# Optimization experiments

Hardware: AMD Instinct MI355X
Metric: run time of the kernel (lower is better)

The kernel has to match this reference:

```python
import jax, jax.numpy as jnp
import numpy as np


def _freq_downsample(x, sf):
    # torch: stack(chunk(dim=2), 4) -> cat(chunk(dim=3), 4) -> mean(-1) -> repeat(1,1,sf,sf)
    # equivalent: mean over the sf x sf grid of contiguous blocks, then tile back.
    B, C, H, W = x.shape
    m = x.reshape(B, C, sf, H // sf, sf, W // sf).mean(axis=(2, 4))
    return jnp.tile(m, (1, 1, sf, sf))


def setup_inputs() -> dict:
    key = jax.random.key(0)
    k1, k2, k3 = jax.random.split(key, 3)
    shape = (4, 3, 256, 256)
    return {
        "STy": jax.random.normal(k1, shape, dtype=jnp.float32),
        "Fk_real": jax.random.normal(k2, shape, dtype=jnp.float32),
        "Fk_imag": jax.random.normal(k3, shape, dtype=jnp.float32),
        "sf": 2,
    }


def _forward(STy, Fk_real, Fk_imag, sf, num_iters=50, alpha=1e-6, gam=0.1):
    fft2 = lambda a: jnp.fft.fft2(a, axes=(-2, -1))
    ifft2 = lambda a: jnp.fft.ifft2(a, axes=(-2, -1))

    Fk = jax.lax.complex(Fk_real, Fk_imag)          # complex64 OTF
    FkC = jnp.conj(Fk)
    Fk2 = Fk_real ** 2 + Fk_imag ** 2               # |Fk|^2, real

    FSTy = fft2(STy)
    Fr = FkC * FSTy / (_freq_downsample(Fk2, sf) + alpha)
    pred = ifft2(Fr).real

    # finite-difference stencils DH = [1,-1] horizontal, DV vertical
    DH = jnp.zeros_like(pred).at[..., 0, 0].set(1.0).at[..., 0, 1].set(-1.0)
    DV = jnp.zeros_like(pred).at[..., 0, 0].set(1.0).at[..., 1, 0].set(-1.0)
    FDH, FDV = fft2(DH), fft2(DV)
    FDHC, FDVC = jnp.conj(FDH), jnp.conj(FDV)
    FD2 = jnp.abs(FDV) ** 2 + jnp.abs(FDH) ** 2 + 1e-8  # real

    # loop-invariant terms (identical math to recomputing each iteration)
    den = _freq_downsample(Fk2 / FD2, sf) + alpha
    FkFSTy = FkC * FSTy

    def body(carry, k):
        pred, x_old, t_old, U1, U2, D1, D2 = carry
        gam_k = gam * jnp.exp2(-k / num_iters)      # gam * 0.5 ** (k/num_iters)
        Fr = FkFSTy + alpha * (FDHC * fft2(U1 - D1) + FDVC * fft2(U2 - D2))
        Fr = (Fr - FkC * _freq_downsample(Fk * Fr / FD2, sf) / den) / (alpha * FD2)
        x_new = ifft2(Fr).real
        t_new = (1.0 + jnp.sqrt(1.0 + 4.0 * t_old ** 2)) / 2.0
        pred = x_new + (t_old - 1.0) / t_new * (x_new - x_old)
        DHr = ifft2(Fr * FDH).real
        DVr = ifft2(Fr * FDV).real
        NU1, NU2 = DHr + D1, DVr + D2
        NU = jnp.sqrt(NU1 ** 2 + NU2 ** 2 + 1e-8)
        A = jnp.maximum(0.0, NU - gam_k) + 1e-8
        A = A / (A + gam_k)                         # soft-threshold magnitude shrink
        U1n, U2n = A * NU1, A * NU2
        return (pred, x_new, t_new, U1n, U2n, D1 + DHr - U1n, D2 + DVr - U2n), None

    carry0 = (pred, pred, jnp.float32(1.0), pred, pred,
              jnp.zeros_like(pred), jnp.zeros_like(pred))
    ks = jnp.arange(num_iters, dtype=jnp.float32)
    (pred, *_), _ = jax.lax.scan(body, carry0, ks)
    return pred


def reference(STy, Fk_real, Fk_imag, sf):
    return _forward(STy, Fk_real, Fk_imag, sf)
```

## Files before the change

kernel.cpp:

```cpp
#include <hip/hip_runtime.h>
#include <math.h>

#define NIMG 12
#define NSZ 256
#define HWSZ 65536

__device__ __forceinline__ void fft256(float2* A, float2* B, const float2* tw, int lane, float dir)
{
  float2* src = A;
  float2* dst = B;
  int m = 1;
#pragma unroll
  for (int s = 0; s < 8; ++s) {
    __syncthreads();
#pragma unroll
    for (int h = 0; h < 2; ++h) {
      int b = lane + (h << 6);
      int k = b & (m - 1);
      int jm = b - k;
      float2 a = src[b];
      float2 c = src[b + 128];
      float2 w = tw[jm];
      float wr = w.x, wi = dir * w.y;
      float ex = a.x - c.x, ey = a.y - c.y;
      dst[2 * jm + k]     = make_float2(a.x + c.x, a.y + c.y);
      dst[2 * jm + k + m] = make_float2(ex * wr - ey * wi, ex * wi + ey * wr);
    }
    float2* t = src; src = dst; dst = t;
    m <<= 1;
  }
  __syncthreads();
}

__device__ __forceinline__ void make_tw(float2* tw, int t)
{
  float s, c;
  sincospif((float)t * (1.0f / 128.0f), &s, &c);
  tw[t] = make_float2(c, s);
}

__device__ __forceinline__ double fdval(const float2* tw, int k)
{
  return 2.0 - 2.0 * (double)tw[k].x;
}

__global__ __launch_bounds__(256) void k_rowfwd_sty(const float* __restrict__ sty,
                                                    float2* __restrict__ Wb)
{
  __shared__ float2 tw[256];
  __shared__ float2 bufA[4][256];
  __shared__ float2 bufB[4][256];
  int t = threadIdx.x;
  make_tw(tw, t);
  int n = blockIdx.x >> 6;
  int r0 = (blockIdx.x & 63) << 2;
  int w = t >> 6, lane = t & 63;
  const float* src = sty + (size_t)n * HWSZ + (size_t)(r0 + w) * NSZ;
#pragma unroll
  for (int q = 0; q < 4; ++q) { int j = lane + (q << 6); bufA[w][j] = make_float2(src[j], 0.f); }
  fft256(bufA[w], bufB[w], tw, lane, -1.f);
  float2* dst = Wb + (size_t)n * HWSZ + (size_t)(r0 + w) * NSZ;
#pragma unroll
  for (int q = 0; q < 4; ++q) { int j = lane + (q << 6); dst[j] = bufA[w][j]; }
}

__global__ __launch_bounds__(256) void k_colsetup(float2* __restrict__ Wb,
                                                  float2* __restrict__ FkF,
                                                  const float* __restrict__ fkr,
                                                  const float* __restrict__ fki,
                                                  float* __restrict__ denq)
{
  __shared__ float2 tw[256];
  __shared__ float2 bufA[4][256];
  __shared__ float2 bufB[4][256];
  __shared__ float dsA[2][128];
  int t = threadIdx.x;
  make_tw(tw, t);
  int n = blockIdx.x >> 6;
  int j0 = (blockIdx.x & 63) << 1;
  int w = t >> 6, lane = t & 63;
  int gcw = j0 + (w & 1) + ((w >> 1) << 7);
  float2* Wn = Wb + (size_t)n * HWSZ;
#pragma unroll
  for (int q = 0; q < 4; ++q) { int u = lane + (q << 6); bufA[w][u] = Wn[(size_t)u * NSZ + gcw]; }
  fft256(bufA[w], bufB[w], tw, lane, -1.f);
#pragma unroll
  for (int c = 0; c < 4; ++c) {
    int u = t;
    int gc = j0 + (c & 1) + ((c >> 1) << 7);
    size_t idx = (size_t)n * HWSZ + (size_t)u * NSZ + gc;
    float kr = fkr[idx], ki = fki[idx];
    float2 f = bufA[c][u];
    float2 kf = make_float2(kr * f.x + ki * f.y, kr * f.y - ki * f.x);
    FkF[idx] = kf;
    bufA[c][u] = kf;
  }
  __syncthreads();
  {
    int u0 = t & 127, p = t >> 7;
    double s1 = 0.0, s2 = 0.0;
#pragma unroll
    for (int s = 0; s < 4; ++s) {
      int u = u0 + ((s & 1) << 7);
      int c = p + ((s >> 1) << 1);
      int gc = j0 + (c & 1) + ((c >> 1) << 7);
      size_t idx = (size_t)n * HWSZ + (size_t)u * NSZ + gc;
      double kr = fkr[idx], ki = fki[idx];
      double k2 = kr * kr + ki * ki;
      double fd2 = fdval(tw, u) + fdval(tw, gc) + 1e-8;
      s1 += k2;
      s2 += k2 / fd2;
    }
    denq[(size_t)n * 16384 + (size_t)u0 * 128 + (j0 + p)] = (float)(s2 * 0.25 + 1e-6);
    dsA[p][u0] = (float)(s1 * 0.25 + 1e-6);
  }
  __syncthreads();
#pragma unroll
  for (int c = 0; c < 4; ++c) {
    int u = t;
    float d = dsA[c & 1][u & 127];
    float2 kf = bufA[c][u];
    bufA[c][u] = make_float2(kf.x / d, kf.y / d);
  }
  fft256(bufA[w], bufB[w], tw, lane, +1.f);
#pragma unroll
  for (int q = 0; q < 4; ++q) { int u = lane + (q << 6); Wn[(size_t)u * NSZ + gcw] = bufA[w][u]; }
}

__global__ __launch_bounds__(256) void k_spatial_rowfwd(const float* __restrict__ x,
                                                        const float* __restrict__ D1p,
                                                        const float* __restrict__ D2p,
                                                        float* __restrict__ D1n,
                                                        float* __restrict__ D2n,
                                                        float2* __restrict__ Wb,
                                                        float gamp, int firstIter)
{
  __shared__ float2 tw[256];
  __shared__ float aL[5][256];
  __shared__ float bL[5][256];
  __shared__ float2 bufA[4][256];
  __shared__ float2 bufB[4][256];
  int t = threadIdx.x;
  make_tw(tw, t);
  int n = blockIdx.x >> 6;
  int r0 = (blockIdx.x & 63) << 2;
  const float* xn = x + (size_t)n * HWSZ;
  for (int rr = 0; rr < 5; ++rr) {
    int i = (r0 + rr) & 255;
    int im1 = (i - 1) & 255;
    int j = t;
    int jm1 = (j - 1) & 255;
    float xc = xn[(size_t)i * NSZ + j];
    float a, b;
    if (firstIter) {
      a = xc; b = xc;
    } else {
      float dhr = xc - xn[(size_t)i * NSZ + jm1];
      float dvr = xc - xn[(size_t)im1 * NSZ + j];
      size_t idx = (size_t)n * HWSZ + (size_t)i * NSZ + j;
      float d1 = D1p[idx], d2 = D2p[idx];
      float nu1 = dhr + d1, nu2 = dvr + d2;
      float nu = sqrtf(nu1 * nu1 + nu2 * nu2 + 1e-8f);
      float A = fmaxf(0.f, nu - gamp) + 1e-8f;
      A = A / (A + gamp);
      float u1 = A * nu1, u2 = A * nu2;
      float d1v = d1 + dhr - u1;
      float d2v = d2 + dvr - u2;
      if (rr < 4) { D1n[idx] = d1v; D2n[idx] = d2v; }
      a = u1 - d1v; b = u2 - d2v;
    }
    aL[rr][j] = a;
    bL[rr][j] = b;
  }
  __syncthreads();
  int w = t >> 6, lane = t & 63;
#pragma unroll
  for (int q = 0; q < 4; ++q) {
    int j = lane + (q << 6);
    int jp1 = (j + 1) & 255;
    float g = aL[w][j] - aL[w][jp1] + bL[w][j] - bL[w + 1][j];
    bufA[w][j] = make_float2(g, 0.f);
  }
  fft256(bufA[w], bufB[w], tw, lane, -1.f);
  float2* dst = Wb + (size_t)n * HWSZ + (size_t)(r0 + w) * NSZ;
#pragma unroll
  for (int q = 0; q < 4; ++q) { int j = lane + (q << 6); dst[j] = bufA[w][j]; }
}

__global__ __launch_bounds__(256) void k_colphase(float2* __restrict__ Wb,
                                                  const float2* __restrict__ FkF,
                                                  const float* __restrict__ fkr,
                                                  const float* __restrict__ fki,
                                                  const float* __restrict__ denq)
{
  __shared__ float2 tw[256];
  __shared__ float2 bufA[4][256];
  __shared__ float2 bufB[4][256];
  __shared__ double2 Ml[2][128];
  int t = threadIdx.x;
  make_tw(tw, t);
  int n = blockIdx.x >> 6;
  int j0 = (blockIdx.x & 63) << 1;
  int w = t >> 6, lane = t & 63;
  int gcw = j0 + (w & 1) + ((w >> 1) << 7);
  float2* Wn = Wb + (size_t)n * HWSZ;
#pragma unroll
  for (int q = 0; q < 4; ++q) { int u = lane + (q << 6); bufA[w][u] = Wn[(size_t)u * NSZ + gcw]; }
  fft256(bufA[w], bufB[w], tw, lane, -1.f);
#pragma unroll
  for (int c = 0; c < 4; ++c) {
    int u = t;
    int gc = j0 + (c & 1) + ((c >> 1) << 7);
    size_t idx = (size_t)n * HWSZ + (size_t)u * NSZ + gc;
    float2 kf = FkF[idx];
    float2 fg = bufA[c][u];
    bufA[c][u] = make_float2(kf.x + 1e-6f * fg.x, kf.y + 1e-6f * fg.y);
  }
  __syncthreads();
  {
    int u0 = t & 127, p = t >> 7;
    double sx = 0.0, sy = 0.0;
#pragma unroll
    for (int s = 0; s < 4; ++s) {
      int u = u0 + ((s & 1) << 7);
      int c = p + ((s >> 1) << 1);
      int gc = j0 + (c & 1) + ((c >> 1) << 7);
      size_t idx = (size_t)n * HWSZ + (size_t)u * NSZ + gc;
      float2 f1 = bufA[c][u];
      double kr = fkr[idx], ki = fki[idx];
      double fd2 = fdval(tw, u) + fdval(tw, gc) + 1e-8;
      sx += (kr * (double)f1.x - ki * (double)f1.y) / fd2;
      sy += (kr * (double)f1.y + ki * (double)f1.x) / fd2;
    }
    Ml[p][u0] = make_double2(sx * 0.25, sy * 0.25);
  }
  __syncthreads();
#pragma unroll
  for (int c = 0; c < 4; ++c) {
    int u = t;
    int gc = j0 + (c & 1) + ((c >> 1) << 7);
    size_t idx = (size_t)n * HWSZ + (size_t)u * NSZ + gc;
    float2 f1 = bufA[c][u];
    double2 m = Ml[c & 1][u & 127];
    double den = (double)denq[(size_t)n * 16384 + (size_t)(u & 127) * 128 + (j0 + (c & 1))];
    double kr = fkr[idx], ki = fki[idx];
    double px = (kr * m.x + ki * m.y) / den;
    double py = (kr * m.y - ki * m.x) / den;
    double fd2 = fdval(tw, u) + fdval(tw, gc) + 1e-8;
    double sc = 1.0 / (1e-6 * fd2);
    bufA[c][u] = make_float2((float)(((double)f1.x - px) * sc),
                             (float)(((double)f1.y - py) * sc));
  }
  fft256(bufA[w], bufB[w], tw, lane, +1.f);
#pragma unroll
  for (int q = 0; q < 4; ++q) { int u = lane + (q << 6); Wn[(size_t)u * NSZ + gcw] = bufA[w][u]; }
}

__global__ __launch_bounds__(256) void k_rowinv(const float2* __restrict__ Wb,
                                                float* __restrict__ xout,
                                                const float* __restrict__ xold,
                                                float* __restrict__ pred,
                                                float cmom, int isLast)
{
  __shared__ float2 tw[256];
  __shared__ float2 bufA[4][256];
  __shared__ float2 bufB[4][256];
  int t = threadIdx.x;
  make_tw(tw, t);
  int n = blockIdx.x >> 6;
  int r0 = (blockIdx.x & 63) << 2;
  int w = t >> 6, lane = t & 63;
  const float2* src = Wb + (size_t)n * HWSZ + (size_t)(r0 + w) * NSZ;
#pragma unroll
  for (int q = 0; q < 4; ++q) { int j = lane + (q << 6); bufA[w][j] = src[j]; }
  fft256(bufA[w], bufB[w], tw, lane, +1.f);
  size_t base = (size_t)n * HWSZ + (size_t)(r0 + w) * NSZ;
#pragma unroll
  for (int q = 0; q < 4; ++q) {
    int j = lane + (q << 6);
    float v = bufA[w][j].x * (1.0f / 65536.0f);
    xout[base + j] = v;
    if (isLast) pred[base + j] = v + cmom * (v - xold[base + j]);
  }
}

extern "C" void kernel_launch(void* const* d_in, const int* in_sizes, int n_in,
                              void* d_out, int out_size, void* d_ws, size_t ws_size,
                              hipStream_t stream)
{
  (void)in_sizes; (void)n_in; (void)out_size; (void)ws_size;
  const float* STy = (const float*)d_in[0];
  const float* fkr = (const float*)d_in[1];
  const float* fki = (const float*)d_in[2];
  float* out = (float*)d_out;

  char* p = (char*)d_ws;
  const size_t cplx = (size_t)NIMG * HWSZ * sizeof(float2);
  const size_t realb = (size_t)NIMG * HWSZ * sizeof(float);
  float2* Wb  = (float2*)p; p += cplx;
  float2* FkF = (float2*)p; p += cplx;
  float* denq = (float*)p;  p += (size_t)NIMG * 16384 * sizeof(float);
  float* D1a = (float*)p;   p += realb;
  float* D2a = (float*)p;   p += realb;
  float* D1b = (float*)p;   p += realb;
  float* D2b = (float*)p;   p += realb;
  float* x0  = (float*)p;   p += realb;
  float* x1  = (float*)p;   p += realb;

  hipMemsetAsync(D1a, 0, 2 * realb, stream);

  dim3 grid(768), blk(256);
  k_rowfwd_sty<<<grid, blk, 0, stream>>>(STy, Wb);
  k_colsetup<<<grid, blk, 0, stream>>>(Wb, FkF, fkr, fki, denq);
  k_rowinv<<<grid, blk, 0, stream>>>(Wb, x0, x0, out, 0.f, 0);

  double t_old = 1.0;
  for (int k = 0; k < 50; ++k) {
    float gamp = (k >= 1) ? (float)(0.1 * exp2(-(double)(k - 1) / 50.0)) : 0.f;
    const float* xk = (k & 1) ? x1 : x0;
    float* xn = (k & 1) ? x0 : x1;
    const float* D1p = (k & 1) ? D1a : D1b;
    const float* D2p = (k & 1) ? D2a : D2b;
    float* D1w = (k & 1) ? D1b : D1a;
    float* D2w = (k & 1) ? D2b : D2a;

    k_spatial_rowfwd<<<grid, blk, 0, stream>>>(xk, D1p, D2p, D1w, D2w, Wb, gamp, (k == 0) ? 1 : 0);
    k_colphase<<<grid, blk, 0, stream>>>(Wb, FkF, fkr, fki, denq);

    double t_new = (1.0 + sqrt(1.0 + 4.0 * t_old * t_old)) * 0.5;
    int isLast = (k == 49) ? 1 : 0;
    float cmom = (float)((t_old - 1.0) / t_new);
    k_rowinv<<<grid, blk, 0, stream>>>(Wb, xn, xk, out, isLast ? cmom : 0.f, isLast);
    t_old = t_new;
  }
}
```

Measured before the change: 2.492 ms.

## Fuse all iterations into one persistent kernel with software grid barriers

Replaces the ~150 separate launches with a single persistent kernel of 768 blocks that uses an atomic-counter grid barrier between the row and column FFT phases. It also merges the inverse row FFT and spatial shrink step into the next forward row FFT by recomputing neighbour rows (halo rows) in shared memory. That removes one global pass and one barrier per iteration. The aim is to cut launch overhead and global memory round trips. The kernel is launched normally rather than cooperatively, so it relies on all 768 blocks being co-resident, which is checked with an occupancy query (3 blocks per CU). The halo rows add redundant FFT work, and the larger shared-memory footprint may limit occupancy.

```diff
diff --git a/kernel.cpp b/kernel.cpp
--- a/kernel.cpp
+++ b/kernel.cpp
@@ -4,8 +4,31 @@
 #define NIMG 12
 #define NSZ 256
 #define HWSZ 65536
-
-__device__ __forceinline__ void fft256(float2* A, float2* B, const float2* tw, int lane, float dir)
+#define NBLK 768
+
+struct GBar { unsigned cnt; unsigned gen; };
+
+__device__ __forceinline__ void gsync(GBar* b)
+{
+  __syncthreads();
+  if (threadIdx.x == 0) {
+    __threadfence();
+    unsigned g = __hip_atomic_load(&b->gen, __ATOMIC_RELAXED, __HIP_MEMORY_SCOPE_AGENT);
+    unsigned a = __hip_atomic_fetch_add(&b->cnt, 1u, __ATOMIC_ACQ_REL, __HIP_MEMORY_SCOPE_AGENT);
+    if (a == NBLK - 1u) {
+      __hip_atomic_store(&b->cnt, 0u, __ATOMIC_RELAXED, __HIP_MEMORY_SCOPE_AGENT);
+      __hip_atomic_store(&b->gen, g + 1u, __ATOMIC_RELEASE, __HIP_MEMORY_SCOPE_AGENT);
+    } else {
+      while (__hip_atomic_load(&b->gen, __ATOMIC_ACQUIRE, __HIP_MEMORY_SCOPE_AGENT) == g)
+        __builtin_amdgcn_s_sleep(2);
+    }
+    __threadfence();
+  }
+  __syncthreads();
+}
+
+__device__ __forceinline__ void fft256g(float2* A, float2* B, const float2* tw, int lane,
+                                        float dir, bool active)
 {
   float2* src = A;
   float2* dst = B;
@@ -13,23 +36,29 @@
 #pragma unroll
   for (int s = 0; s < 8; ++s) {
     __syncthreads();
-#pragma unroll
-    for (int h = 0; h < 2; ++h) {
-      int b = lane + (h << 6);
-      int k = b & (m - 1);
-      int jm = b - k;
-      float2 a = src[b];
-      float2 c = src[b + 128];
-      float2 w = tw[jm];
-      float wr = w.x, wi = dir * w.y;
-      float ex = a.x - c.x, ey = a.y - c.y;
-      dst[2 * jm + k]     = make_float2(a.x + c.x, a.y + c.y);
-      dst[2 * jm + k + m] = make_float2(ex * wr - ey * wi, ex * wi + ey * wr);
+    if (active) {
+#pragma unroll
+      for (int h = 0; h < 2; ++h) {
+        int b = lane + (h << 6);
+        int k = b & (m - 1);
+        int jm = b - k;
+        float2 a = src[b];
+        float2 c = src[b + 128];
+        float2 w = tw[jm];
+        float wr = w.x, wi = dir * w.y;
+        float ex = a.x - c.x, ey = a.y - c.y;
+        dst[2 * jm + k]     = make_float2(a.x + c.x, a.y + c.y);
+        dst[2 * jm + k + m] = make_float2(ex * wr - ey * wi, ex * wi + ey * wr);
+      }
     }
     float2* t = src; src = dst; dst = t;
     m <<= 1;
   }
   __syncthreads();
+}
+__device__ __forceinline__ void fft256(float2* A, float2* B, const float2* tw, int lane, float dir)
+{
+  fft256g(A, B, tw, lane, dir, true);
 }
 
 __device__ __forceinline__ void make_tw(float2* tw, int t)
@@ -42,6 +71,239 @@
 __device__ __forceinline__ double fdval(const float2* tw, int k)
 {
   return 2.0 - 2.0 * (double)tw[k].x;
+}
+
+__global__ __launch_bounds__(256, 3) void k_mega(const float* __restrict__ sty,
+                                                 const float* __restrict__ fkr,
+                                                 const float* __restrict__ fki,
+                                                 float2* __restrict__ WG,
+                                                 float2* __restrict__ WF,
+                                                 float2* __restrict__ FkF,
+                                                 float* __restrict__ denq,
+                                                 float* D1a, float* D2a,
+                                                 float* D1b, float* D2b,
+                                                 float* __restrict__ x49,
+                                                 float* __restrict__ out,
+                                                 float cmom, GBar* bar)
+{
+  __shared__ float2 tw[256];
+  __shared__ float2 bufA[6][256];
+  __shared__ float2 bufB[6][256];
+  __shared__ float aL[5][256];
+  __shared__ float bL[5][256];
+  __shared__ float dsA[2][128];
+  __shared__ double2 Ml[2][128];
+
+  int t = threadIdx.x;
+  make_tw(tw, t);
+  int bid = blockIdx.x;
+  int n = bid >> 6;
+  int sr = bid & 63;
+  int r0 = sr << 2;
+  int j0 = sr << 1;
+  int w = t >> 6, lane = t & 63;
+  const float sc = 1.0f / 65536.0f;
+  int gcw = j0 + (w & 1) + ((w >> 1) << 7);
+
+  {
+    const float* src = sty + (size_t)n * HWSZ + (size_t)(r0 + w) * NSZ;
+#pragma unroll
+    for (int q = 0; q < 4; ++q) { int j = lane + (q << 6); bufA[w][j] = make_float2(src[j], 0.f); }
+    fft256(bufA[w], bufB[w], tw, lane, -1.f);
+    float2* dst = WG + (size_t)n * HWSZ + (size_t)(r0 + w) * NSZ;
+#pragma unroll
+    for (int q = 0; q < 4; ++q) { int j = lane + (q << 6); dst[j] = bufA[w][j]; }
+  }
+  gsync(bar);
+
+  {
+    float2* WGn = WG + (size_t)n * HWSZ;
+#pragma unroll
+    for (int q = 0; q < 4; ++q) { int u = lane + (q << 6); bufA[w][u] = WGn[(size_t)u * NSZ + gcw]; }
+    fft256(bufA[w], bufB[w], tw, lane, -1.f);
+#pragma unroll
+    for (int c = 0; c < 4; ++c) {
+      int u = t;
+      int gc = j0 + (c & 1) + ((c >> 1) << 7);
+      size_t idx = (size_t)n * HWSZ + (size_t)u * NSZ + gc;
+      float kr = fkr[idx], ki = fki[idx];
+      float2 f = bufA[c][u];
+      float2 kf = make_float2(kr * f.x + ki * f.y, kr * f.y - ki * f.x);
+      FkF[idx] = kf;
+      bufA[c][u] = kf;
+    }
+    __syncthreads();
+    {
+      int u0 = t & 127, p = t >> 7;
+      double s1 = 0.0, s2 = 0.0;
+#pragma unroll
+      for (int s = 0; s < 4; ++s) {
+        int u = u0 + ((s & 1) << 7);
+        int c = p + ((s >> 1) << 1);
+        int gc = j0 + (c & 1) + ((c >> 1) << 7);
+        size_t idx = (size_t)n * HWSZ + (size_t)u * NSZ + gc;
+        double kr = fkr[idx], ki = fki[idx];
+        double k2 = kr * kr + ki * ki;
+        double fd2 = fdval(tw, u) + fdval(tw, gc) + 1e-8;
+        s1 += k2;
+        s2 += k2 / fd2;
+      }
+      denq[(size_t)n * 16384 + (size_t)u0 * 128 + (j0 + p)] = (float)(s2 * 0.25 + 1e-6);
+      dsA[p][u0] = (float)(s1 * 0.25 + 1e-6);
+    }
+    __syncthreads();
+#pragma unroll
+    for (int c = 0; c < 4; ++c) {
+      int u = t;
+      float d = dsA[c & 1][u & 127];
+      float2 kf = bufA[c][u];
+      bufA[c][u] = make_float2(kf.x / d, kf.y / d);
+    }
+    fft256(bufA[w], bufB[w], tw, lane, +1.f);
+    float2* WFn = WF + (size_t)n * HWSZ;
+#pragma unroll
+    for (int q = 0; q < 4; ++q) { int u = lane + (q << 6); WFn[(size_t)u * NSZ + gcw] = bufA[w][u]; }
+  }
+  gsync(bar);
+
+  for (int k = 0; k < 50; ++k) {
+    float gamp = (k >= 1) ? (float)(0.1 * exp2(-(double)(k - 1) / 50.0)) : 0.f;
+    const float *D1p, *D2p; float *D1w, *D2w;
+    if (k & 1) { D1p = D1a; D2p = D2a; D1w = D1b; D2w = D2b; }
+    else       { D1p = D1b; D2p = D2b; D1w = D1a; D2w = D2a; }
+
+    {
+      int gr = (r0 + w - 1) & 255;
+      const float2* srcW = WF + (size_t)n * HWSZ + (size_t)gr * NSZ;
+#pragma unroll
+      for (int q = 0; q < 4; ++q) { int j = lane + (q << 6); bufA[w][j] = srcW[j]; }
+      fft256(bufA[w], bufB[w], tw, lane, +1.f);
+    }
+    {
+      bool act = (w < 2);
+      int e = 4 + (w & 1);
+      int gr = (r0 + e - 1) & 255;
+      if (act) {
+        const float2* srcW = WF + (size_t)n * HWSZ + (size_t)gr * NSZ;
+#pragma unroll
+        for (int q = 0; q < 4; ++q) { int j = lane + (q << 6); bufA[e][j] = srcW[j]; }
+      }
+      fft256g(bufA[e], bufB[e], tw, lane, +1.f, act);
+    }
+    for (int e = 1; e <= 5; ++e) {
+      int gr = (r0 + e - 1) & 255;
+      int j = t, jm1 = (j - 1) & 255;
+      float xc = bufA[e][j].x * sc;
+      size_t idx = (size_t)n * HWSZ + (size_t)gr * NSZ + j;
+      if (k == 49 && e <= 4) x49[idx] = xc;
+      float a, b;
+      if (k == 0) {
+        a = xc; b = xc;
+      } else {
+        float xl = bufA[e][jm1].x * sc;
+        float xu = bufA[e - 1][j].x * sc;
+        float dhr = xc - xl;
+        float dvr = xc - xu;
+        float d1 = D1p[idx], d2 = D2p[idx];
+        float nu1 = dhr + d1, nu2 = dvr + d2;
+        float nu = sqrtf(nu1 * nu1 + nu2 * nu2 + 1e-8f);
+        float A = fmaxf(0.f, nu - gamp) + 1e-8f;
+        A = A / (A + gamp);
+        float u1 = A * nu1, u2 = A * nu2;
+        float d1v = d1 + dhr - u1;
+        float d2v = d2 + dvr - u2;
+        if (e <= 4) { D1w[idx] = d1v; D2w[idx] = d2v; }
+        a = u1 - d1v; b = u2 - d2v;
+      }
+      aL[e - 1][j] = a;
+      bL[e - 1][j] = b;
+    }
+    __syncthreads();
+    {
+#pragma unroll
+      for (int q = 0; q < 4; ++q) {
+        int j = lane + (q << 6);
+        int jp1 = (j + 1) & 255;
+        float g = aL[w][j] - aL[w][jp1] + bL[w][j] - bL[w + 1][j];
+        bufA[w][j] = make_float2(g, 0.f);
+      }
+      fft256(bufA[w], bufB[w], tw, lane, -1.f);
+      float2* dst = WG + (size_t)n * HWSZ + (size_t)(r0 + w) * NSZ;
+#pragma unroll
+      for (int q = 0; q < 4; ++q) { int j = lane + (q << 6); dst[j] = bufA[w][j]; }
+    }
+    gsync(bar);
+
+    {
+      float2* WGn = WG + (size_t)n * HWSZ;
+#pragma unroll
+      for (int q = 0; q < 4; ++q) { int u = lane + (q << 6); bufA[w][u] = WGn[(size_t)u * NSZ + gcw]; }
+      fft256(bufA[w], bufB[w], tw, lane, -1.f);
+#pragma unroll
+      for (int c = 0; c < 4; ++c) {
+        int u = t;
+        int gc = j0 + (c & 1) + ((c >> 1) << 7);
+        size_t idx = (size_t)n * HWSZ + (size_t)u * NSZ + gc;
+        float2 kf = FkF[idx];
+        float2 fg = bufA[c][u];
+        bufA[c][u] = make_float2(kf.x + 1e-6f * fg.x, kf.y + 1e-6f * fg.y);
+      }
+      __syncthreads();
+      {
+        int u0 = t & 127, p = t >> 7;
+        double sx = 0.0, sy = 0.0;
+#pragma unroll
+        for (int s = 0; s < 4; ++s) {
+          int u = u0 + ((s & 1) << 7);
+          int c = p + ((s >> 1) << 1);
+          int gc = j0 + (c & 1) + ((c >> 1) << 7);
+          size_t idx = (size_t)n * HWSZ + (size_t)u * NSZ + gc;
+          float2 f1 = bufA[c][u];
+          double kr = fkr[idx], ki = fki[idx];
+          double fd2 = fdval(tw, u) + fdval(tw, gc) + 1e-8;
+          sx += (kr * (double)f1.x - ki * (double)f1.y) / fd2;
+          sy += (kr * (double)f1.y + ki * (double)f1.x) / fd2;
+        }
+        Ml[p][u0] = make_double2(sx * 0.25, sy * 0.25);
+      }
+      __syncthreads();
+#pragma unroll
+      for (int c = 0; c < 4; ++c) {
+        int u = t;
+        int gc = j0 + (c & 1) + ((c >> 1) << 7);
+        size_t idx = (size_t)n * HWSZ + (size_t)u * NSZ + gc;
+        float2 f1 = bufA[c][u];
+        double2 m = Ml[c & 1][u & 127];
+        double den = (double)denq[(size_t)n * 16384 + (size_t)(u & 127) * 128 + (j0 + (c & 1))];
+        double kr = fkr[idx], ki = fki[idx];
+        double px = (kr * m.x + ki * m.y) / den;
+        double py = (kr * m.y - ki * m.x) / den;
+        double fd2 = fdval(tw, u) + fdval(tw, gc) + 1e-8;
+        double s2 = 1.0 / (1e-6 * fd2);
+        bufA[c][u] = make_float2((float)(((double)f1.x - px) * s2),
+                                 (float)(((double)f1.y - py) * s2));
+      }
+      fft256(bufA[w], bufB[w], tw, lane, +1.f);
+      float2* WFn = WF + (size_t)n * HWSZ;
+#pragma unroll
+      for (int q = 0; q < 4; ++q) { int u = lane + (q << 6); WFn[(size_t)u * NSZ + gcw] = bufA[w][u]; }
+    }
+    gsync(bar);
+  }
+
+  {
+    const float2* srcW = WF + (size_t)n * HWSZ + (size_t)(r0 + w) * NSZ;
+#pragma unroll
+    for (int q = 0; q < 4; ++q) { int j = lane + (q << 6); bufA[w][j] = srcW[j]; }
+    fft256(bufA[w], bufB[w], tw, lane, +1.f);
+    size_t base = (size_t)n * HWSZ + (size_t)(r0 + w) * NSZ;
+#pragma unroll
+    for (int q = 0; q < 4; ++q) {
+      int j = lane + (q << 6);
+      float v = bufA[w][j].x * sc;
+      out[base + j] = v + cmom * (v - x49[base + j]);
+    }
+  }
 }
 
 __global__ __launch_bounds__(256) void k_rowfwd_sty(const float* __restrict__ sty,
@@ -247,9 +509,9 @@
     double px = (kr * m.x + ki * m.y) / den;
     double py = (kr * m.y - ki * m.x) / den;
     double fd2 = fdval(tw, u) + fdval(tw, gc) + 1e-8;
-    double sc = 1.0 / (1e-6 * fd2);
-    bufA[c][u] = make_float2((float)(((double)f1.x - px) * sc),
-                             (float)(((double)f1.y - py) * sc));
+    double s2 = 1.0 / (1e-6 * fd2);
+    bufA[c][u] = make_float2((float)(((double)f1.x - px) * s2),
+                             (float)(((double)f1.y - py) * s2));
   }
   fft256(bufA[w], bufB[w], tw, lane, +1.f);
 #pragma unroll
@@ -297,40 +559,58 @@
   char* p = (char*)d_ws;
   const size_t cplx = (size_t)NIMG * HWSZ * sizeof(float2);
   const size_t realb = (size_t)NIMG * HWSZ * sizeof(float);
-  float2* Wb  = (float2*)p; p += cplx;
+  float2* WG  = (float2*)p; p += cplx;
+  float2* WF  = (float2*)p; p += cplx;
   float2* FkF = (float2*)p; p += cplx;
   float* denq = (float*)p;  p += (size_t)NIMG * 16384 * sizeof(float);
   float* D1a = (float*)p;   p += realb;
   float* D2a = (float*)p;   p += realb;
   float* D1b = (float*)p;   p += realb;
   float* D2b = (float*)p;   p += realb;
-  float* x0  = (float*)p;   p += realb;
-  float* x1  = (float*)p;   p += realb;
+  float* xA  = (float*)p;   p += realb;
+  float* xB  = (float*)p;   p += realb;
+  GBar* bar  = (GBar*)p;    p += 64;
+
+  double t_old = 1.0, cm = 0.0;
+  for (int k = 0; k < 50; ++k) {
+    double t_new = (1.0 + sqrt(1.0 + 4.0 * t_old * t_old)) * 0.5;
+    if (k == 49) cm = (t_old - 1.0) / t_new;
+    t_old = t_new;
+  }
+
+  int maxb = 0;
+  hipError_t oe = hipOccupancyMaxActiveBlocksPerMultiprocessor(&maxb, k_mega, 256, 0);
+  bool coop = (oe == hipSuccess && maxb >= 3);
 
   hipMemsetAsync(D1a, 0, 2 * realb, stream);
 
-  dim3 grid(768), blk(256);
-  k_rowfwd_sty<<<grid, blk, 0, stream>>>(STy, Wb);
-  k_colsetup<<<grid, blk, 0, stream>>>(Wb, FkF, fkr, fki, denq);
-  k_rowinv<<<grid, blk, 0, stream>>>(Wb, x0, x0, out, 0.f, 0);
-
-  double t_old = 1.0;
-  for (int k = 0; k < 50; ++k) {
-    float gamp = (k >= 1) ? (float)(0.1 * exp2(-(double)(k - 1) / 50.0)) : 0.f;
-    const float* xk = (k & 1) ? x1 : x0;
-    float* xn = (k & 1) ? x0 : x1;
-    const float* D1p = (k & 1) ? D1a : D1b;
-    const float* D2p = (k & 1) ? D2a : D2b;
-    float* D1w = (k & 1) ? D1b : D1a;
-    float* D2w = (k & 1) ? D2b : D2a;
-
-    k_spatial_rowfwd<<<grid, blk, 0, stream>>>(xk, D1p, D2p, D1w, D2w, Wb, gamp, (k == 0) ? 1 : 0);
-    k_colphase<<<grid, blk, 0, stream>>>(Wb, FkF, fkr, fki, denq);
-
-    double t_new = (1.0 + sqrt(1.0 + 4.0 * t_old * t_old)) * 0.5;
-    int isLast = (k == 49) ? 1 : 0;
-    float cmom = (float)((t_old - 1.0) / t_new);
-    k_rowinv<<<grid, blk, 0, stream>>>(Wb, xn, xk, out, isLast ? cmom : 0.f, isLast);
-    t_old = t_new;
-  }
-}
+  dim3 grid(NBLK), blk(256);
+  if (coop) {
+    hipMemsetAsync(bar, 0, sizeof(GBar), stream);
+    k_mega<<<grid, blk, 0, stream>>>(STy, fkr, fki, WG, WF, FkF, denq,
+                                     D1a, D2a, D1b, D2b, xA, out, (float)cm, bar);
+  } else {
+    float2* Wb = WG;
+    float* x0 = xA; float* x1 = xB;
+    k_rowfwd_sty<<<grid, blk, 0, stream>>>(STy, Wb);
+    k_colsetup<<<grid, blk, 0, stream>>>(Wb, FkF, fkr, fki, denq);
+    k_rowinv<<<grid, blk, 0, stream>>>(Wb, x0, x0, out, 0.f, 0);
+    double to = 1.0;
+    for (int k = 0; k < 50; ++k) {
+      float gamp = (k >= 1) ? (float)(0.1 * exp2(-(double)(k - 1) / 50.0)) : 0.f;
+      const float* xk = (k & 1) ? x1 : x0;
+      float* xn = (k & 1) ? x0 : x1;
+      const float* D1p = (k & 1) ? D1a : D1b;
+      const float* D2p = (k & 1) ? D2a : D2b;
+      float* D1w = (k & 1) ? D1b : D1a;
+      float* D2w = (k & 1) ? D2b : D2a;
+      k_spatial_rowfwd<<<grid, blk, 0, stream>>>(xk, D1p, D2p, D1w, D2w, Wb, gamp, (k == 0) ? 1 : 0);
+      k_colphase<<<grid, blk, 0, stream>>>(Wb, FkF, fkr, fki, denq);
+      double tn = (1.0 + sqrt(1.0 + 4.0 * to * to)) * 0.5;
+      int isLast = (k == 49) ? 1 : 0;
+      float cmom = (float)((to - 1.0) / tn);
+      k_rowinv<<<grid, blk, 0, stream>>>(Wb, xn, xk, out, isLast ? cmom : 0.f, isLast);
+      to = tn;
+    }
+  }
+}
```

Result: no change. 2.499 ms (+0.3%).
